# Kernel optimization log

Hardware: AMD Instinct MI355X
Metric: run time of the kernel (lower is better)

## Reference

```python
import jax, jax.numpy as jnp
import numpy as np

IN_DIM = 256
OUT_DIM = 256
NUM_HEADS = 4
HEAD_DIM = OUT_DIM // NUM_HEADS
N_SRC = 100000
N_DST = 50000
N_EDGES = 300000


def setup_inputs() -> dict:
    key = jax.random.key(0)
    ks = jax.random.split(key, 10)
    h_src = jax.random.normal(ks[0], (N_SRC, IN_DIM), dtype=jnp.float32)
    h_dst = jax.random.normal(ks[1], (N_DST, IN_DIM), dtype=jnp.float32)
    src_idx = jax.random.randint(ks[2], (N_EDGES,), 0, N_SRC)
    dst_idx = jax.random.randint(ks[3], (N_EDGES,), 0, N_DST)
    # torch nn.Linear weights are [out, in]; xavier-uniform init, zero bias
    def xavier(k, shape):
        limit = jnp.sqrt(6.0 / (shape[0] + shape[1]))
        return jax.random.uniform(k, shape, jnp.float32, -limit, limit)
    Wq = xavier(ks[4], (OUT_DIM, IN_DIM))
    Wk = xavier(ks[5], (OUT_DIM, IN_DIM))
    Wv = xavier(ks[6], (OUT_DIM, IN_DIM))
    bq = jnp.zeros((OUT_DIM,), jnp.float32)
    bk = jnp.zeros((OUT_DIM,), jnp.float32)
    bv = jnp.zeros((OUT_DIM,), jnp.float32)
    return {"h_src": h_src, "h_dst": h_dst, "src_idx": src_idx, "dst_idx": dst_idx,
            "Wq": Wq, "bq": bq, "Wk": Wk, "bk": bk, "Wv": Wv, "bv": bv}


def reference(h_src, h_dst, src_idx, dst_idx, Wq, bq, Wk, bk, Wv, bv):
    # Projections (torch Linear: x @ W.T + b), reshape to [N, H, Dh]
    Q = (h_dst @ Wq.T + bq).reshape(-1, NUM_HEADS, HEAD_DIM)
    K = (h_src @ Wk.T + bk).reshape(-1, NUM_HEADS, HEAD_DIM)
    V = (h_src @ Wv.T + bv).reshape(-1, NUM_HEADS, HEAD_DIM)

    # Edge scores: u_dot_v('K','Q') -> per-edge, per-head dot product [E, H]
    score = jnp.einsum('ehd,ehd->eh', K[src_idx], Q[dst_idx]) / jnp.sqrt(
        jnp.asarray(HEAD_DIM, jnp.float32))

    # Edge softmax grouped by destination (per head), numerically stable
    seg_max = jax.ops.segment_max(score, dst_idx, num_segments=N_DST)
    seg_max = jnp.where(jnp.isfinite(seg_max), seg_max, 0.0)
    e = jnp.exp(score - seg_max[dst_idx])
    seg_sum = jax.ops.segment_sum(e, dst_idx, num_segments=N_DST)
    a = e / seg_sum[dst_idx]  # [E, H]

    # Weighted sum aggregation: u_mul_e then sum per destination
    m = V[src_idx] * a[:, :, None]  # [E, H, Dh]
    h = jax.ops.segment_sum(m, dst_idx, num_segments=N_DST)  # [N_dst, H, Dh]
    return h.reshape(-1, OUT_DIM)
```

## Files before the change

### kernel.cpp

```cpp
#include <hip/hip_runtime.h>
#include <hip/hip_bf16.h>
#include <stdint.h>

#define IN_DIM    256
#define OUT_DIM   256
#define NUM_HEADS 4
#define HEAD_DIM  64
#define N_SRC     100000
#define N_DST     50000
#define N_EDGES   300000

#define BM 128
#define BN 256
#define BK 32
#define SCAN_NBLK ((N_DST + 1023) / 1024)
#define WCVT_BLKS 96

typedef __attribute__((ext_vector_type(8))) short v8s;
typedef __attribute__((ext_vector_type(4))) float v4f;

__device__ __forceinline__ unsigned short f2bf(float f) {
    unsigned u = __float_as_uint(f);
    unsigned r = (u + 0x7FFFu + ((u >> 16) & 1u)) >> 16;
    return (unsigned short)r;
}
__device__ __forceinline__ float bf2f(unsigned short s) {
    return __uint_as_float(((unsigned)s) << 16);
}

__device__ __forceinline__ void async_copy16(const unsigned short* g,
                                             unsigned short* l) {
    __builtin_amdgcn_global_load_lds(
        (const __attribute__((address_space(1))) unsigned int*)g,
        (__attribute__((address_space(3))) unsigned int*)l, 16, 0, 0);
}

__global__ void wcvt_kernel(const float* __restrict__ wq,
                            const float* __restrict__ wk,
                            const float* __restrict__ wv,
                            unsigned short* __restrict__ dst,
                            int* __restrict__ cnt) {
    if (blockIdx.x >= WCVT_BLKS) {
        int i = (blockIdx.x - WCVT_BLKS) * 1024 + threadIdx.x * 4;
        if (i < N_DST) *(int4*)(cnt + i) = make_int4(0, 0, 0, 0);
        return;
    }
    int i = blockIdx.x * 256 + threadIdx.x;
    if (i >= 3 * 8192) return;
    int m = i >> 13;
    int r = i & 8191;
    const float* s = (m == 0) ? wq : (m == 1) ? wk : wv;
    const float4* sp = (const float4*)(s + (size_t)r * 8);
    float4 x = sp[0], y = sp[1];
    v8s o;
    o[0] = (short)f2bf(x.x); o[1] = (short)f2bf(x.y);
    o[2] = (short)f2bf(x.z); o[3] = (short)f2bf(x.w);
    o[4] = (short)f2bf(y.x); o[5] = (short)f2bf(y.y);
    o[6] = (short)f2bf(y.z); o[7] = (short)f2bf(y.w);
    *(v8s*)(dst + (size_t)m * 65536 + (size_t)r * 8) = o;
}

__global__ __launch_bounds__(1024, 5) void gemm_kernel(
    const float* __restrict__ h_src, const float* __restrict__ h_dst,
    const unsigned short* __restrict__ Wb,
    const float* __restrict__ bq, const float* __restrict__ bk,
    const float* __restrict__ bv,
    unsigned short* __restrict__ Q, unsigned short* __restrict__ K,
    unsigned short* __restrict__ V) {

    __shared__ unsigned short smem[24576];

    int z = blockIdx.z;
    const float* A; const unsigned short* W;
    const float* bias; unsigned short* Out; int M;
    if (z == 0)      { A = h_dst; W = Wb;          bias = bq; Out = Q; M = N_DST; }
    else if (z == 1) { A = h_src; W = Wb + 65536;  bias = bk; Out = K; M = N_SRC; }
    else             { A = h_src; W = Wb + 131072; bias = bv; Out = V; M = N_SRC; }

    int mbase = blockIdx.x * BM;
    if (mbase >= M) return;

    int tid  = threadIdx.x;
    int wave = tid >> 6, lane = tid & 63;
    int lm = lane & 15, quad = lane >> 4;
    int wrow = wave >> 3;
    int wcol = wave & 7;

    int ar = tid >> 3, akc = (tid & 7) * 4;
    int gr = mbase + ar; if (gr > M - 1) gr = M - 1;
    const float* gA = A + (size_t)gr * 256 + akc;

    int sr = lane >> 2, skc = (lane & 3) * 8;
    const unsigned short* gB0 = W + (size_t)(wave * 16 + sr) * 256 + skc;

    v4f acc[4][2];
#pragma unroll
    for (int i = 0; i < 4; i++)
#pragma unroll
        for (int j = 0; j < 2; j++) acc[i][j] = (v4f){0, 0, 0, 0};

    const int NK = 256 / BK;

    float4 xc;
    {
        float4 x0 = *(const float4*)(gA);
        async_copy16(gB0, &smem[8192 + (wave * 16) * 32]);
        __builtin_amdgcn_sched_barrier(0);
        xc = *(const float4*)(gA + BK);
        ushort4 o;
        o.x = f2bf(x0.x); o.y = f2bf(x0.y);
        o.z = f2bf(x0.z); o.w = f2bf(x0.w);
        *(ushort4*)&smem[(size_t)ar * 32 + akc] = o;
        asm volatile("s_waitcnt vmcnt(1) lgkmcnt(0)" ::: "memory");
        __builtin_amdgcn_s_barrier();
        __builtin_amdgcn_sched_barrier(0);
    }

    int buf = 0;
#pragma unroll
    for (int ks = 0; ks < NK; ks++) {
        float4 xn;
        if (ks + 1 < NK) {
            async_copy16(gB0 + (ks + 1) * BK,
                         &smem[8192 + (buf ^ 1) * 8192 + (wave * 16) * 32]);
        }
        __builtin_amdgcn_sched_barrier(0);
        if (ks + 2 < NK) {
            xn = *(const float4*)(gA + (ks + 2) * BK);
        }

        const unsigned short* sAb = smem + buf * 4096;
        const unsigned short* sBb = smem + 8192 + buf * 8192;
        v8s af[4], bfr[2];
#pragma unroll
        for (int i = 0; i < 4; i++)
            af[i] = *(const v8s*)&sAb[(wrow * 64 + i * 16 + lm) * 32 + quad * 8];
#pragma unroll
        for (int j = 0; j < 2; j++)
            bfr[j] = *(const v8s*)&sBb[(wcol * 32 + j * 16 + lm) * 32 + quad * 8];
#pragma unroll
        for (int i = 0; i < 4; i++)
#pragma unroll
            for (int j = 0; j < 2; j++)
                acc[i][j] = __builtin_amdgcn_mfma_f32_16x16x32_bf16(
                    af[i], bfr[j], acc[i][j], 0, 0, 0);

        if (ks + 1 < NK) {
            ushort4 o;
            o.x = f2bf(xc.x); o.y = f2bf(xc.y);
            o.z = f2bf(xc.z); o.w = f2bf(xc.w);
            *(ushort4*)&smem[(buf ^ 1) * 4096 + (size_t)ar * 32 + akc] = o;
        }
        if (ks <= 5)
            asm volatile("s_waitcnt vmcnt(1) lgkmcnt(0)" ::: "memory");
        else if (ks == 6)
            asm volatile("s_waitcnt vmcnt(0) lgkmcnt(0)" ::: "memory");
        if (ks < NK - 1) {
            __builtin_amdgcn_s_barrier();
            __builtin_amdgcn_sched_barrier(0);
        }
        xc = xn;
        buf ^= 1;
    }

#pragma unroll
    for (int p = 0; p < 2; p++) {
        __syncthreads();
        if (wrow == p) {
#pragma unroll
            for (int j = 0; j < 2; j++) {
                int col = wcol * 32 + j * 16 + lm;
                float bcol = bias[col];
#pragma unroll
                for (int i = 0; i < 4; i++)
#pragma unroll
                    for (int r = 0; r < 4; r++)
                        smem[(i * 16 + quad * 4 + r) * 256 + col] =
                            f2bf(acc[i][j][r] + bcol);
            }
        }
        __syncthreads();
#pragma unroll
        for (int k = 0; k < 2; k++) {
            int c = tid + k * 1024;
            int rl = c >> 5, ch = c & 31;
            int grow = mbase + p * 64 + rl;
            if (grow < M)
                *(v8s*)(Out + (size_t)grow * 256 + ch * 8) =
                    *(const v8s*)&smem[rl * 256 + ch * 8];
        }
    }
}

__global__ void hist_kernel(const int* __restrict__ dst_idx,
                            int* __restrict__ cnt) {
    int i = blockIdx.x * 256 + threadIdx.x;
    if (i < N_EDGES) atomicAdd(&cnt[dst_idx[i]], 1);
}

__global__ __launch_bounds__(1024) void scan_local_kernel(
    const int* __restrict__ cnt, int* __restrict__ offsets,
    int* __restrict__ cursor, int* __restrict__ bsum) {
    __shared__ int wsum[16];
    int t = threadIdx.x, b = blockIdx.x;
    int i = b * 1024 + t;
    int lane = t & 63, w = t >> 6;
    int v = (i < N_DST) ? cnt[i] : 0;
    int s = v;
#pragma unroll
    for (int off = 1; off < 64; off <<= 1) {
        int u = __shfl_up(s, off, 64);
        if (lane >= off) s += u;
    }
    if (lane == 63) wsum[w] = s;
    __syncthreads();
    if (w == 0) {
        int x = (lane < 16) ? wsum[lane] : 0;
#pragma unroll
        for (int off = 1; off < 16; off <<= 1) {
            int u = __shfl_up(x, off, 64);
            if (lane >= off) x += u;
        }
        if (lane < 16) wsum[lane] = x;
    }
    __syncthreads();
    int wbase = (w == 0) ? 0 : wsum[w - 1];
    if (i < N_DST) {
        int e = wbase + s - v;
        offsets[i] = e;
        cursor[i] = e;
    }
    if (t == 1023) bsum[b] = wsum[15];
}

__global__ void scan_base_kernel(int* __restrict__ bsum) {
    int lane = threadIdx.x;
    int v = (lane < SCAN_NBLK) ? bsum[lane] : 0;
    int s = v;
#pragma unroll
    for (int off = 1; off < 64; off <<= 1) {
        int u = __shfl_up(s, off, 64);
        if (lane >= off) s += u;
    }
    if (lane < SCAN_NBLK) bsum[lane] = s - v;
}

__global__ void scatter_kernel(const int* __restrict__ src_idx,
                               const int* __restrict__ dst_idx,
                               int* __restrict__ cursor,
                               const int* __restrict__ bsum,
                               int* __restrict__ esrc) {
    int i = blockIdx.x * 256 + threadIdx.x;
    if (i >= N_EDGES) return;
    int d = dst_idx[i];
    int pos = atomicAdd(&cursor[d], 1) + bsum[d >> 10];
    esrc[pos] = src_idx[i];
}

__global__ __launch_bounds__(256) void agg_kernel(
    const int* __restrict__ esrc, const int* __restrict__ offsets,
    const int* __restrict__ bsum,
    const unsigned short* __restrict__ Q, const unsigned short* __restrict__ K,
    const unsigned short* __restrict__ V, float* __restrict__ out) {

    int wave = threadIdx.x >> 6, lane = threadIdx.x & 63;
    int d = blockIdx.x * 4 + wave;
    if (d >= N_DST) return;

    int start = offsets[d] + bsum[d >> 10];
    int end = (d + 1 == N_DST) ? N_EDGES
                               : offsets[d + 1] + bsum[(d + 1) >> 10];
    float4 o = make_float4(0.f, 0.f, 0.f, 0.f);

    if (end > start) {
        ushort4 qv = *((const ushort4*)(Q + (size_t)d * 256) + lane);
        float q0 = bf2f(qv.x), q1 = bf2f(qv.y), q2 = bf2f(qv.z), q3 = bf2f(qv.w);

        float m = -3.0e38f, l = 0.f;
        float a0 = 0.f, a1 = 0.f, a2 = 0.f, a3 = 0.f;

        int s0 = esrc[start];
        int sN = (start + 1 < end) ? esrc[start + 1] : 0;
        ushort4 kv = *((const ushort4*)(K + (size_t)s0 * 256) + lane);
        ushort4 vv = *((const ushort4*)(V + (size_t)s0 * 256) + lane);

        for (int j = start; j < end; j++) {
            ushort4 kc = kv, vc = vv;
            int sNN = (j + 2 < end) ? esrc[j + 2] : 0;
            if (j + 1 < end) {
                kv = *((const ushort4*)(K + (size_t)sN * 256) + lane);
                vv = *((const ushort4*)(V + (size_t)sN * 256) + lane);
            }
            sN = sNN;

            float p = bf2f(kc.x) * q0 + bf2f(kc.y) * q1 +
                      bf2f(kc.z) * q2 + bf2f(kc.w) * q3;
            p += __shfl_xor(p, 1, 64);
            p += __shfl_xor(p, 2, 64);
            p += __shfl_xor(p, 4, 64);
            p += __shfl_xor(p, 8, 64);
            p *= 0.125f;

            float mn = fmaxf(m, p);
            float sc = __expf(m - mn);
            float w  = __expf(p - mn);
            l = l * sc + w;
            a0 = a0 * sc + w * bf2f(vc.x);
            a1 = a1 * sc + w * bf2f(vc.y);
            a2 = a2 * sc + w * bf2f(vc.z);
            a3 = a3 * sc + w * bf2f(vc.w);
            m = mn;
        }
        float inv = 1.0f / l;
        o = make_float4(a0 * inv, a1 * inv, a2 * inv, a3 * inv);
    }
    *((float4*)(out + (size_t)d * 256) + lane) = o;
}

extern "C" void kernel_launch(void* const* d_in, const int* in_sizes, int n_in,
                              void* d_out, int out_size, void* d_ws, size_t ws_size,
                              hipStream_t stream) {
    const float* h_src   = (const float*)d_in[0];
    const float* h_dst   = (const float*)d_in[1];
    const int*   src_idx = (const int*)d_in[2];
    const int*   dst_idx = (const int*)d_in[3];
    const float* Wq      = (const float*)d_in[4];
    const float* bq      = (const float*)d_in[5];
    const float* Wk      = (const float*)d_in[6];
    const float* bk      = (const float*)d_in[7];
    const float* Wv      = (const float*)d_in[8];
    const float* bv      = (const float*)d_in[9];
    float* out = (float*)d_out;

    char* ws = (char*)d_ws;
    size_t off = 0;
    auto take = [&](size_t bytes) { char* p = ws + off; off = (off + bytes + 255) & ~(size_t)255; return p; };
    unsigned short* Q       = (unsigned short*)take((size_t)N_DST * 256 * 2);
    unsigned short* K       = (unsigned short*)take((size_t)N_SRC * 256 * 2);
    unsigned short* V       = (unsigned short*)take((size_t)N_SRC * 256 * 2);
    unsigned short* Wb      = (unsigned short*)take((size_t)3 * 65536 * 2);
    int*            cnt     = (int*)take((size_t)N_DST * 4);
    int*            offsets = (int*)take((size_t)(N_DST + 1) * 4);
    int*            cursor  = (int*)take((size_t)N_DST * 4);
    int*            esrc    = (int*)take((size_t)N_EDGES * 4);
    int*            bsum    = (int*)take((size_t)64 * 4);
    (void)ws_size; (void)in_sizes; (void)n_in; (void)out_size;

    wcvt_kernel<<<WCVT_BLKS + SCAN_NBLK, 256, 0, stream>>>(Wq, Wk, Wv, Wb, cnt);

    hist_kernel<<<(N_EDGES + 255) / 256, 256, 0, stream>>>(dst_idx, cnt);
    scan_local_kernel<<<SCAN_NBLK, 1024, 0, stream>>>(cnt, offsets, cursor, bsum);
    scan_base_kernel<<<1, 64, 0, stream>>>(bsum);
    scatter_kernel<<<(N_EDGES + 255) / 256, 256, 0, stream>>>(src_idx, dst_idx,
                                                              cursor, bsum, esrc);

    gemm_kernel<<<dim3((N_SRC + BM - 1) / BM, 1, 3), 1024, 0, stream>>>(
        h_src, h_dst, Wb, bq, bk, bv, Q, K, V);

    agg_kernel<<<(N_DST + 3) / 4, 256, 0, stream>>>(esrc, offsets, bsum, Q, K, V, out);
}
```

Baseline: 359.8 us.

## Replace LDS-staged GEMM with register-direct MFMA loads on smaller tiles

The projection GEMM no longer stages A and W tiles through shared memory with async copies and barriers. Each wave now loads its MFMA fragments straight from global memory into registers, double-buffered, and converts A to bf16 in registers. Blocks shrink to 256 threads with 64x128 output tiles, and the grid is split over N. This removes LDS traffic and barriers, but each A row is now read once per N-half instead of once per block, and the direct global fragment loads are strided and less coalesced.

```diff
diff --git a/kernel.cpp b/kernel.cpp
--- a/kernel.cpp
+++ b/kernel.cpp
@@ -10,9 +10,6 @@
 #define N_DST     50000
 #define N_EDGES   300000
 
-#define BM 128
-#define BN 256
-#define BK 32
 #define SCAN_NBLK ((N_DST + 1023) / 1024)
 #define WCVT_BLKS 96
 
@@ -26,13 +23,6 @@
 }
 __device__ __forceinline__ float bf2f(unsigned short s) {
     return __uint_as_float(((unsigned)s) << 16);
-}
-
-__device__ __forceinline__ void async_copy16(const unsigned short* g,
-                                             unsigned short* l) {
-    __builtin_amdgcn_global_load_lds(
-        (const __attribute__((address_space(1))) unsigned int*)g,
-        (__attribute__((address_space(3))) unsigned int*)l, 16, 0, 0);
 }
 
 __global__ void wcvt_kernel(const float* __restrict__ wq,
@@ -60,7 +50,7 @@
     *(v8s*)(dst + (size_t)m * 65536 + (size_t)r * 8) = o;
 }
 
-__global__ __launch_bounds__(1024, 5) void gemm_kernel(
+__global__ __launch_bounds__(256, 3) void gemm_kernel(
     const float* __restrict__ h_src, const float* __restrict__ h_dst,
     const unsigned short* __restrict__ Wb,
     const float* __restrict__ bq, const float* __restrict__ bk,
@@ -68,7 +58,7 @@
     unsigned short* __restrict__ Q, unsigned short* __restrict__ K,
     unsigned short* __restrict__ V) {
 
-    __shared__ unsigned short smem[24576];
+    __shared__ unsigned short smem[64 * 128];
 
     int z = blockIdx.z;
     const float* A; const unsigned short* W;
@@ -77,21 +67,25 @@
     else if (z == 1) { A = h_src; W = Wb + 65536;  bias = bk; Out = K; M = N_SRC; }
     else             { A = h_src; W = Wb + 131072; bias = bv; Out = V; M = N_SRC; }
 
-    int mbase = blockIdx.x * BM;
-    if (mbase >= M) return;
-
-    int tid  = threadIdx.x;
-    int wave = tid >> 6, lane = tid & 63;
+    int pbase = blockIdx.x * 64;
+    if (pbase >= M) return;
+    int nbase = blockIdx.y * 128;
+
+    int tid = threadIdx.x;
+    int wv = tid >> 6, lane = tid & 63;
     int lm = lane & 15, quad = lane >> 4;
-    int wrow = wave >> 3;
-    int wcol = wave & 7;
-
-    int ar = tid >> 3, akc = (tid & 7) * 4;
-    int gr = mbase + ar; if (gr > M - 1) gr = M - 1;
-    const float* gA = A + (size_t)gr * 256 + akc;
-
-    int sr = lane >> 2, skc = (lane & 3) * 8;
-    const unsigned short* gB0 = W + (size_t)(wave * 16 + sr) * 256 + skc;
+
+    const float* pA[4];
+#pragma unroll
+    for (int i = 0; i < 4; i++) {
+        int gr = pbase + i * 16 + lm;
+        if (gr > M - 1) gr = M - 1;
+        pA[i] = A + (size_t)gr * 256 + quad * 8;
+    }
+    const unsigned short* pB[2];
+#pragma unroll
+    for (int j = 0; j < 2; j++)
+        pB[j] = W + (size_t)(nbase + wv * 32 + j * 16 + lm) * 256 + quad * 8;
 
     v4f acc[4][2];
 #pragma unroll
@@ -99,96 +93,69 @@
 #pragma unroll
         for (int j = 0; j < 2; j++) acc[i][j] = (v4f){0, 0, 0, 0};
 
-    const int NK = 256 / BK;
-
-    float4 xc;
-    {
-        float4 x0 = *(const float4*)(gA);
-        async_copy16(gB0, &smem[8192 + (wave * 16) * 32]);
-        __builtin_amdgcn_sched_barrier(0);
-        xc = *(const float4*)(gA + BK);
-        ushort4 o;
-        o.x = f2bf(x0.x); o.y = f2bf(x0.y);
-        o.z = f2bf(x0.z); o.w = f2bf(x0.w);
-        *(ushort4*)&smem[(size_t)ar * 32 + akc] = o;
-        asm volatile("s_waitcnt vmcnt(1) lgkmcnt(0)" ::: "memory");
-        __builtin_amdgcn_s_barrier();
-        __builtin_amdgcn_sched_barrier(0);
-    }
-
-    int buf = 0;
-#pragma unroll
-    for (int ks = 0; ks < NK; ks++) {
-        float4 xn;
-        if (ks + 1 < NK) {
-            async_copy16(gB0 + (ks + 1) * BK,
-                         &smem[8192 + (buf ^ 1) * 8192 + (wave * 16) * 32]);
+    float4 abuf[2][4][2];
+    v8s    bbuf[2][2];
+
+#pragma unroll
+    for (int i = 0; i < 4; i++) {
+        abuf[0][i][0] = *(const float4*)(pA[i]);
+        abuf[0][i][1] = *(const float4*)(pA[i] + 4);
+    }
+#pragma unroll
+    for (int j = 0; j < 2; j++) bbuf[0][j] = *(const v8s*)(pB[j]);
+
+#pragma unroll
+    for (int ks = 0; ks < 8; ks++) {
+        int cur = ks & 1, nxt = cur ^ 1;
+        if (ks + 1 < 8) {
+#pragma unroll
+            for (int i = 0; i < 4; i++) {
+                abuf[nxt][i][0] = *(const float4*)(pA[i] + (ks + 1) * 32);
+                abuf[nxt][i][1] = *(const float4*)(pA[i] + (ks + 1) * 32 + 4);
+            }
+#pragma unroll
+            for (int j = 0; j < 2; j++)
+                bbuf[nxt][j] = *(const v8s*)(pB[j] + (ks + 1) * 32);
         }
-        __builtin_amdgcn_sched_barrier(0);
-        if (ks + 2 < NK) {
-            xn = *(const float4*)(gA + (ks + 2) * BK);
+        v8s af[4];
+#pragma unroll
+        for (int i = 0; i < 4; i++) {
+            float4 lo = abuf[cur][i][0], hi = abuf[cur][i][1];
+            v8s o;
+            o[0] = (short)f2bf(lo.x); o[1] = (short)f2bf(lo.y);
+            o[2] = (short)f2bf(lo.z); o[3] = (short)f2bf(lo.w);
+            o[4] = (short)f2bf(hi.x); o[5] = (short)f2bf(hi.y);
+            o[6] = (short)f2bf(hi.z); o[7] = (short)f2bf(hi.w);
+            af[i] = o;
         }
-
-        const unsigned short* sAb = smem + buf * 4096;
-        const unsigned short* sBb = smem + 8192 + buf * 8192;
-        v8s af[4], bfr[2];
-#pragma unroll
-        for (int i = 0; i < 4; i++)
-            af[i] = *(const v8s*)&sAb[(wrow * 64 + i * 16 + lm) * 32 + quad * 8];
-#pragma unroll
-        for (int j = 0; j < 2; j++)
-            bfr[j] = *(const v8s*)&sBb[(wcol * 32 + j * 16 + lm) * 32 + quad * 8];
 #pragma unroll
         for (int i = 0; i < 4; i++)
 #pragma unroll
             for (int j = 0; j < 2; j++)
                 acc[i][j] = __builtin_amdgcn_mfma_f32_16x16x32_bf16(
-                    af[i], bfr[j], acc[i][j], 0, 0, 0);
-
-        if (ks + 1 < NK) {
-            ushort4 o;
-            o.x = f2bf(xc.x); o.y = f2bf(xc.y);
-            o.z = f2bf(xc.z); o.w = f2bf(xc.w);
-            *(ushort4*)&smem[(buf ^ 1) * 4096 + (size_t)ar * 32 + akc] = o;
-        }
-        if (ks <= 5)
-            asm volatile("s_waitcnt vmcnt(1) lgkmcnt(0)" ::: "memory");
-        else if (ks == 6)
-            asm volatile("s_waitcnt vmcnt(0) lgkmcnt(0)" ::: "memory");
-        if (ks < NK - 1) {
-            __builtin_amdgcn_s_barrier();
-            __builtin_amdgcn_sched_barrier(0);
-        }
-        xc = xn;
-        buf ^= 1;
-    }
-
-#pragma unroll
-    for (int p = 0; p < 2; p++) {
-        __syncthreads();
-        if (wrow == p) {
-#pragma unroll
-            for (int j = 0; j < 2; j++) {
-                int col = wcol * 32 + j * 16 + lm;
-                float bcol = bias[col];
-#pragma unroll
-                for (int i = 0; i < 4; i++)
-#pragma unroll
-                    for (int r = 0; r < 4; r++)
-                        smem[(i * 16 + quad * 4 + r) * 256 + col] =
-                            f2bf(acc[i][j][r] + bcol);
-            }
-        }
-        __syncthreads();
-#pragma unroll
-        for (int k = 0; k < 2; k++) {
-            int c = tid + k * 1024;
-            int rl = c >> 5, ch = c & 31;
-            int grow = mbase + p * 64 + rl;
-            if (grow < M)
-                *(v8s*)(Out + (size_t)grow * 256 + ch * 8) =
-                    *(const v8s*)&smem[rl * 256 + ch * 8];
-        }
+                    af[i], bbuf[cur][j], acc[i][j], 0, 0, 0);
+    }
+
+#pragma unroll
+    for (int j = 0; j < 2; j++) {
+        int col = wv * 32 + j * 16 + lm;
+        float bcol = bias[nbase + col];
+#pragma unroll
+        for (int i = 0; i < 4; i++)
+#pragma unroll
+            for (int r = 0; r < 4; r++)
+                smem[(i * 16 + quad * 4 + r) * 128 + col] =
+                    f2bf(acc[i][j][r] + bcol);
+    }
+    __syncthreads();
+#pragma unroll
+    for (int k = 0; k < 4; k++) {
+        int c = tid + k * 256;
+        int rl = c >> 4, ch = c & 15;
+        int grow = pbase + rl;
+        if (grow < M)
+            *(v8s*)(Out + (size_t)grow * 256 + nbase + ch * 8) =
+                *(const v8s*)&smem[rl * 128 + ch * 8];
     }
 }
 
@@ -354,7 +321,7 @@
     scatter_kernel<<<(N_EDGES + 255) / 256, 256, 0, stream>>>(src_idx, dst_idx,
                                                               cursor, bsum, esrc);
 
-    gemm_kernel<<<dim3((N_SRC + BM - 1) / BM, 1, 3), 1024, 0, stream>>>(
+    gemm_kernel<<<dim3((N_SRC + 63) / 64, 2, 3), 256, 0, stream>>>(
         h_src, h_dst, Wb, bq, bk, bv, Q, K, V);
 
     agg_kernel<<<(N_DST + 3) / 4, 256, 0, stream>>>(esrc, offsets, bsum, Q, K, V, out);
```

Measured after the change: 545.7 us. +51.6%, slower.
